# Kernel tuning notes

Measured on AMD Instinct MI355X. Metric: run time of the kernel, lower is better.

## Reference

```python
import jax, jax.numpy as jnp
import numpy as np

SOBEL = np.array([[1, 0, -1], [2, 0, -2], [1, 0, -1]], dtype=np.float32)


def _conv3(x, w):
    # 3x3 conv, stride 1, padding 1, no bias (NCHW / OIHW)
    return jax.lax.conv_general_dilated(
        x, w, window_strides=(1, 1), padding='SAME',
        dimension_numbers=('NCHW', 'OIHW', 'NCHW'))


def _sobel_conv(x, wx, wy, w1, b1):
    # |sobel_x| + |sobel_y| followed by 1x1 conv (w1: [O, C])
    e = jnp.abs(_conv3(x, wx)) + jnp.abs(_conv3(x, wy))
    return jnp.einsum('bchw,oc->bohw', e, w1) + b1[None, :, None, None]


def setup_inputs() -> dict:
    key = jax.random.key(0)
    ks = jax.random.split(key, 12)
    B, C, H, W = 2, 64, 64, 64
    dk = C // 8
    sob = jnp.asarray(SOBEL)
    inp = {
        'vi': jax.random.normal(ks[0], (B, C, H, W), jnp.float32),
        'ir': jax.random.normal(ks[1], (B, C, H, W), jnp.float32),
        # Sobel conv weights: torch copy_ broadcasts the 3x3 kernel over [C,C,3,3]
        'wsx_vi': jnp.broadcast_to(sob, (C, C, 3, 3)).copy(),
        'wsy_vi': jnp.broadcast_to(sob.T, (C, C, 3, 3)).copy(),
        'w1_vi': jax.random.normal(ks[2], (dk, C), jnp.float32) * 0.05,
        'b1_vi': jax.random.normal(ks[3], (dk,), jnp.float32) * 0.05,
        'wsx_q': jnp.broadcast_to(sob, (2 * C, 2 * C, 3, 3)).copy(),
        'wsy_q': jnp.broadcast_to(sob.T, (2 * C, 2 * C, 3, 3)).copy(),
        'w1_q': jax.random.normal(ks[4], (dk, 2 * C), jnp.float32) * 0.05,
        'b1_q': jax.random.normal(ks[5], (dk,), jnp.float32) * 0.05,
        'wsx_ir': jnp.broadcast_to(sob, (C, C, 3, 3)).copy(),
        'wsy_ir': jnp.broadcast_to(sob.T, (C, C, 3, 3)).copy(),
        'w1_ir': jax.random.normal(ks[6], (dk, C), jnp.float32) * 0.05,
        'b1_ir': jax.random.normal(ks[7], (dk,), jnp.float32) * 0.05,
        'wv_vi': jax.random.normal(ks[8], (C, C), jnp.float32) * 0.05,
        'bv_vi': jax.random.normal(ks[9], (C,), jnp.float32) * 0.05,
        'wv_ir': jax.random.normal(ks[10], (C, C), jnp.float32) * 0.05,
        'bv_ir': jax.random.normal(ks[11], (C,), jnp.float32) * 0.05,
    }
    return inp


def reference(vi, ir, wsx_vi, wsy_vi, w1_vi, b1_vi, wsx_q, wsy_q, w1_q, b1_q,
              wsx_ir, wsy_ir, w1_ir, b1_ir, wv_vi, bv_vi, wv_ir, bv_ir):
    B, C, H, W = vi.shape
    N = H * W
    # Query from concatenated modalities: [B, N, dk]
    xq = _sobel_conv(jnp.concatenate([vi, ir], axis=1), wsx_q, wsy_q, w1_q, b1_q)
    xq = xq.reshape(B, -1, N).transpose(0, 2, 1)
    # Keys: [B, dk, N]
    vi_xk = _sobel_conv(vi, wsx_vi, wsy_vi, w1_vi, b1_vi).reshape(B, -1, N)
    ir_xk = _sobel_conv(ir, wsx_ir, wsy_ir, w1_ir, b1_ir).reshape(B, -1, N)
    # Values (1x1 convs): [B, C, N]
    vi_xv = (jnp.einsum('bchw,oc->bohw', vi, wv_vi) + bv_vi[None, :, None, None]).reshape(B, C, N)
    ir_xv = (jnp.einsum('bchw,oc->bohw', ir, wv_ir) + bv_ir[None, :, None, None]).reshape(B, C, N)
    # Unscaled attention, softmax over last dim: [B, N, N]
    vi_attn = jax.nn.softmax(jnp.einsum('bnd,bdm->bnm', xq, vi_xk), axis=-1)
    ir_attn = jax.nn.softmax(jnp.einsum('bnd,bdm->bnm', xq, ir_xk), axis=-1)
    # Cross combination: vi value routed by ir attention (and vice versa)
    vi_out = jnp.einsum('bcn,bmn->bcm', vi_xv, ir_attn).reshape(B, C, H, W)
    ir_out = jnp.einsum('bcn,bmn->bcm', ir_xv, vi_attn).reshape(B, C, H, W)
    return vi_out, ir_out
```

## Files before the change

kernel.cpp:

```cpp
#include <hip/hip_runtime.h>
#include <hip/hip_bf16.h>

typedef __attribute__((ext_vector_type(8))) short bf16x8;
typedef __attribute__((ext_vector_type(4))) float f32x4;
typedef __attribute__((ext_vector_type(4))) int   i32x4;


__global__ __launch_bounds__(256) void kP_prep(
    const float* __restrict__ vi, const float* __restrict__ ir,
    const float* __restrict__ w1_vi, const float* __restrict__ w1_q,
    const float* __restrict__ b1_q,  const float* __restrict__ w1_ir,
    const float* __restrict__ wv_vi, const float* __restrict__ bv_vi,
    const float* __restrict__ wv_ir, const float* __restrict__ bv_ir,
    float* __restrict__ s, float* __restrict__ scal,
    __hip_bfloat16* __restrict__ Vc) {
    const int t = threadIdx.x;
    if (blockIdx.x < 256) {
        __shared__ __align__(16) char wlds[64 * 128];
        const int bm = blockIdx.x >> 6, nt = blockIdx.x & 63;
        const int b = bm >> 1, mod = bm & 1;
        const float* wv = mod ? wv_ir : wv_vi;
        const float* bv = mod ? bv_ir : bv_vi;
        const float* x = (mod ? ir : vi) + b * (64 * 4096);
        {
            const float* src = wv + t * 16;
            int row = t >> 2, colb = (t & 3) * 32;
            int pk[8];
            #pragma unroll
            for (int j = 0; j < 8; ++j)
                asm("v_cvt_pk_bf16_f32 %0, %1, %2" : "=v"(pk[j])
                    : "v"(src[2 * j]), "v"(src[2 * j + 1]));
            int sw = (row & 7) << 4;
            i32x4 lo = {pk[0], pk[1], pk[2], pk[3]};
            i32x4 hi = {pk[4], pk[5], pk[6], pk[7]};
            *(i32x4*)(wlds + row * 128 + (colb ^ sw)) = lo;
            *(i32x4*)(wlds + row * 128 + ((colb + 16) ^ sw)) = hi;
        }
        __syncthreads();
        const int wvid = t >> 6, lane = t & 63;
        const int col = lane & 15, g = lane >> 4;
        const int n = nt * 64 + wvid * 16 + col;
        bf16x8 afr[4][2];
        #pragma unroll
        for (int cb = 0; cb < 4; ++cb) {
            int row = cb * 16 + col;
            int sw = (row & 7) << 4;
            #pragma unroll
            for (int ks = 0; ks < 2; ++ks)
                afr[cb][ks] = *(const bf16x8*)(wlds + row * 128 + ((ks * 64 + g * 16) ^ sw));
        }
        float ssum = 0.f;
        bf16x8 bfr[2];
        #pragma unroll
        for (int ks = 0; ks < 2; ++ks) {
            const float* xr = x + (ks * 32 + g * 8) * 4096 + n;
            float v[8];
            #pragma unroll
            for (int j = 0; j < 8; ++j) { v[j] = xr[j * 4096]; ssum += v[j]; }
            int pk[4];
            #pragma unroll
            for (int j = 0; j < 4; ++j)
                asm("v_cvt_pk_bf16_f32 %0, %1, %2" : "=v"(pk[j])
                    : "v"(v[2 * j]), "v"(v[2 * j + 1]));
            i32x4 bi = {pk[0], pk[1], pk[2], pk[3]};
            bfr[ks] = __builtin_bit_cast(bf16x8, bi);
        }
        ssum += __shfl_xor(ssum, 16);
        ssum += __shfl_xor(ssum, 32);
        if (lane < 16) s[bm * 4096 + nt * 64 + wvid * 16 + lane] = ssum;

        f32x4 acc[4];
        #pragma unroll
        for (int cb = 0; cb < 4; ++cb)
            #pragma unroll
            for (int r = 0; r < 4; ++r) acc[cb][r] = bv[cb * 16 + g * 4 + r];
        #pragma unroll
        for (int ks = 0; ks < 2; ++ks)
            #pragma unroll
            for (int cb = 0; cb < 4; ++cb)
                acc[cb] = __builtin_amdgcn_mfma_f32_16x16x32_bf16(afr[cb][ks], bfr[ks], acc[cb], 0, 0, 0);
        __hip_bfloat16* outp = Vc + (size_t)(bm * 64) * 4096 + n;
        #pragma unroll
        for (int cb = 0; cb < 4; ++cb)
            #pragma unroll
            for (int r = 0; r < 4; ++r)
                outp[(cb * 16 + g * 4 + r) * 4096] = __float2bfloat16(acc[cb][r]);
    } else {
        __shared__ float Ad[8], Cv[8], Ci[8], Bq[8];
        if (t < 8) {
            float a = 0.f;
            for (int c = 0; c < 128; ++c) a += w1_q[t * 128 + c];
            float cv = 0.f, ci = 0.f;
            for (int c = 0; c < 64; ++c) { cv += w1_vi[t * 64 + c]; ci += w1_ir[t * 64 + c]; }
            Ad[t] = a; Cv[t] = cv; Ci[t] = ci; Bq[t] = b1_q[t];
        }
        __syncthreads();
        if (t == 0) {
            float av = 0, gv = 0, ai = 0, gi = 0;
            for (int d = 0; d < 8; ++d) {
                av += Ad[d] * Cv[d]; gv += Bq[d] * Cv[d];
                ai += Ad[d] * Ci[d]; gi += Bq[d] * Ci[d];
            }
            scal[0] = av; scal[1] = gv; scal[2] = ai; scal[3] = gi;
        }
    }
}

#define CH 512
#define NCH 8
__global__ __launch_bounds__(512, 2) void k4_attn(
        const float* __restrict__ s, const float* __restrict__ scal,
        const float* __restrict__ wsx_vi, const float* __restrict__ wsy_vi,
        const float* __restrict__ wsx_q,  const float* __restrict__ wsy_q,
        const float* __restrict__ wsx_ir, const float* __restrict__ wsy_ir,
        const __hip_bfloat16* __restrict__ Vc, float* __restrict__ out) {
    __shared__ __align__(16) char vbuf[2][64 * CH * 2];
    __shared__ __align__(16) float elds[4096];
    __shared__ float mm[16];
    const int mt = blockIdx.x;
    const int bw = blockIdx.y;
    const int b = bw >> 1, which = bw & 1;
    const int amod = which ? 0 : 1;
    const float* wsxa = amod ? wsx_ir : wsx_vi;
    const float* wsya = amod ? wsy_ir : wsy_vi;
    const float alpha = scal[which ? 0 : 2];
    const float gamma = scal[which ? 1 : 3];
    const short* Vg = (const short*)(Vc + (size_t)(bw * 64) * 4096);

    const int tid = threadIdx.x;
    const int wvw = tid >> 6, lane = tid & 63;
    const int h = wvw >> 2, wvt = wvw & 3;
    const int col = lane & 15, g = lane >> 4;
    const int m = mt * 64 + wvt * 16 + col;

    float* sld = (float*)vbuf[0];
    const float* sg = s + (size_t)(b * 2) * 4096;
    #pragma unroll
    for (int k = 0; k < 16; ++k) { int i = tid + k * 512; sld[i] = sg[i]; }
    __syncthreads();

    float mn = 3.0e38f, mx = 0.f;
    {
        const float* sa = sld + amod * 4096;
        #pragma unroll
        for (int k2 = 0; k2 < 8; ++k2) {
            int n = tid + k2 * 512;
            int hh = n >> 6, ww = n & 63;
            float gx = 0.f, gy = 0.f;
            #pragma unroll
            for (int di = 0; di < 3; ++di)
                #pragma unroll
                for (int dj = 0; dj < 3; ++dj) {
                    int r = hh + di - 1, c2 = ww + dj - 1;
                    bool in = (r >= 0) & (r < 64) & (c2 >= 0) & (c2 < 64);
                    float v = in ? sa[r * 64 + c2] : 0.f;
                    int kk = di * 3 + dj;
                    gx = fmaf(v, wsxa[kk], gx);
                    gy = fmaf(v, wsya[kk], gy);
                }
            float ev = fabsf(gx) + fabsf(gy);
            elds[n] = ev;
            mn = fminf(mn, ev); mx = fmaxf(mx, ev);
        }
    }
    float eq;
    {
        int ww = wvt * 16 + col;
        float gx = 0.f, gy = 0.f;
        #pragma unroll
        for (int di = 0; di < 3; ++di)
            #pragma unroll
            for (int dj = 0; dj < 3; ++dj) {
                int r = mt + di - 1, c2 = ww + dj - 1;
                bool in = (r >= 0) & (r < 64) & (c2 >= 0) & (c2 < 64);
                float v = in ? (sld[r * 64 + c2] + sld[4096 + r * 64 + c2]) : 0.f;
                int kk = di * 3 + dj;
                gx = fmaf(v, wsx_q[kk], gx);
                gy = fmaf(v, wsy_q[kk], gy);
            }
        eq = fabsf(gx) + fabsf(gy);
    }
    #pragma unroll
    for (int o = 32; o; o >>= 1) {
        mn = fminf(mn, __shfl_xor(mn, o));
        mx = fmaxf(mx, __shfl_xor(mx, o));
    }
    if (lane == 0) { mm[wvw] = mn; mm[8 + wvw] = mx; }
    __syncthreads();
    float emn = mm[0], emx = mm[8];
    #pragma unroll
    for (int w = 1; w < 8; ++w) {
        emn = fminf(emn, mm[w]); emx = fmaxf(emx, mm[8 + w]);
    }
    const float L2E = 1.4426950408889634f;
    const float t  = alpha * eq + gamma;
    const float t2 = t * L2E;
    const float nM2 = -((t > 0.f) ? t * emx : t * emn) * L2E;

    #pragma unroll
    for (int k = 0; k < 8; ++k) {
        int id = tid + k * 512;
        int c = id >> 6, ss = id & 63;
        bf16x8 v = *(const bf16x8*)(Vg + c * 4096 + ss * 8);
        *(bf16x8*)(vbuf[0] + c * 1024 + ((ss * 16) ^ ((c & 31) << 4))) = v;
    }
    __syncthreads();

    f32x4 acc[4] = {};
    f32x4 accz = {};
    bf16x8 ones;
    #pragma unroll
    for (int j = 0; j < 8; ++j) ones[j] = (short)0x3F80;

    for (int ck = 0; ck < NCH; ++ck) {
        bf16x8 stg[8];
        const bool pf = (ck + 1 < NCH);
        if (pf) {
            const short* src = Vg + (ck + 1) * CH;
            #pragma unroll
            for (int k = 0; k < 8; ++k) {
                int id = tid + k * 512;
                int c = id >> 6, ss = id & 63;
                stg[k] = *(const bf16x8*)(src + c * 4096 + ss * 8);
            }
        }
        const char* vb = vbuf[ck & 1];
        const float* el = elds + ck * CH;
        #pragma unroll
        for (int it2 = 0; it2 < 8; ++it2) {
            const int n0 = (h * 8 + it2) * 32;
            bf16x8 af[4];
            #pragma unroll
            for (int cb = 0; cb < 4; ++cb) {
                int row = cb * 16 + col;
                int byte = row * 1024 + (((n0 + g * 8) * 2) ^ ((row & 31) << 4));
                af[cb] = *(const bf16x8*)(vb + byte);
            }
            f32x4 e0 = *(const f32x4*)(el + n0 + g * 8);
            f32x4 e1 = *(const f32x4*)(el + n0 + g * 8 + 4);
            float p[8];
            #pragma unroll
            for (int j = 0; j < 4; ++j) {
                float g0 = fmaf(e0[j], t2, nM2);
                float g1 = fmaf(e1[j], t2, nM2);
                asm("v_exp_f32 %0, %1" : "=v"(p[j])     : "v"(g0));
                asm("v_exp_f32 %0, %1" : "=v"(p[j + 4]) : "v"(g1));
            }
            int pk0, pk1, pk2, pk3;
            asm("v_cvt_pk_bf16_f32 %0, %1, %2" : "=v"(pk0) : "v"(p[0]), "v"(p[1]));
            asm("v_cvt_pk_bf16_f32 %0, %1, %2" : "=v"(pk1) : "v"(p[2]), "v"(p[3]));
            asm("v_cvt_pk_bf16_f32 %0, %1, %2" : "=v"(pk2) : "v"(p[4]), "v"(p[5]));
            asm("v_cvt_pk_bf16_f32 %0, %1, %2" : "=v"(pk3) : "v"(p[6]), "v"(p[7]));
            i32x4 pki = {pk0, pk1, pk2, pk3};
            bf16x8 bfrag = __builtin_bit_cast(bf16x8, pki);
            #pragma unroll
            for (int cb = 0; cb < 4; ++cb)
                acc[cb] = __builtin_amdgcn_mfma_f32_16x16x32_bf16(af[cb], bfrag, acc[cb], 0, 0, 0);
            accz = __builtin_amdgcn_mfma_f32_16x16x32_bf16(ones, bfrag, accz, 0, 0, 0);
        }
        __syncthreads();
        if (pf) {
            char* wb = vbuf[(ck + 1) & 1];
            #pragma unroll
            for (int k = 0; k < 8; ++k) {
                int id = tid + k * 512;
                int c = id >> 6, ss = id & 63;
                *(bf16x8*)(wb + c * 1024 + ((ss * 16) ^ ((c & 31) << 4))) = stg[k];
            }
            __syncthreads();
        }
    }

    float* red = (float*)vbuf[0];
    if (h == 1) {
        int base = (wvt * 64 + lane) * 21;
        #pragma unroll
        for (int cb = 0; cb < 4; ++cb)
            *(f32x4*)(red + base + cb * 4) = acc[cb];
        red[base + 16] = accz[0];
    }
    __syncthreads();
    if (h == 0) {
        int base = (wvt * 64 + lane) * 21;
        #pragma unroll
        for (int cb = 0; cb < 4; ++cb)
            acc[cb] += *(const f32x4*)(red + base + cb * 4);
        float z = accz[0] + red[base + 16];
        float inv = 1.0f / z;
        float* ob = out + which * (2 * 64 * 4096) + b * (64 * 4096) + m;
        #pragma unroll
        for (int cb = 0; cb < 4; ++cb) {
            int c = cb * 16 + g * 4;
            #pragma unroll
            for (int r = 0; r < 4; ++r) ob[(c + r) * 4096] = acc[cb][r] * inv;
        }
    }
}

extern "C" void kernel_launch(void* const* d_in, const int* in_sizes, int n_in,
                              void* d_out, int out_size, void* d_ws, size_t ws_size,
                              hipStream_t stream) {
    const float* vi     = (const float*)d_in[0];
    const float* ir     = (const float*)d_in[1];
    const float* wsx_vi = (const float*)d_in[2];
    const float* wsy_vi = (const float*)d_in[3];
    const float* w1_vi  = (const float*)d_in[4];
    const float* wsx_q  = (const float*)d_in[6];
    const float* wsy_q  = (const float*)d_in[7];
    const float* w1_q   = (const float*)d_in[8];
    const float* b1_q   = (const float*)d_in[9];
    const float* wsx_ir = (const float*)d_in[10];
    const float* wsy_ir = (const float*)d_in[11];
    const float* w1_ir  = (const float*)d_in[12];
    const float* wv_vi  = (const float*)d_in[14];
    const float* bv_vi  = (const float*)d_in[15];
    const float* wv_ir  = (const float*)d_in[16];
    const float* bv_ir  = (const float*)d_in[17];
    (void)in_sizes; (void)n_in; (void)out_size;

    char* ws = (char*)d_ws;
    float* scal = (float*)ws;
    float* s    = (float*)(ws + 1280);
    __hip_bfloat16* Vc = (__hip_bfloat16*)(ws + 1280 + 65536);
    float* out = (float*)d_out;
    (void)ws_size;

    kP_prep<<<dim3(257), 256, 0, stream>>>(vi, ir, w1_vi, w1_q, b1_q, w1_ir,
                                           wv_vi, bv_vi, wv_ir, bv_ir, s, scal, Vc);
    k4_attn<<<dim3(64, 4), 512, 0, stream>>>(s, scal, wsx_vi, wsy_vi, wsx_q, wsy_q,
                                             wsx_ir, wsy_ir, Vc, out);
}
```

Measured before the change: 34.46 us.

## Fuse prep and attention kernels into one cooperative launch with grid sync

Merges the prep kernel (value projection, channel sums, scalar reductions) and the attention kernel into a single cooperative kernel of 256 blocks separated by a grid-wide barrier. Each block also recomputes the alpha/gamma scalars locally from w1 sums in shared memory instead of reading them from a separate workspace. The aim is to remove one kernel launch and the gap between launches. In exchange it adds grid-sync overhead, and the cooperative launch requires all 256 blocks to be resident at once.

Result: slower. 67.52 us (+96.0%).

```diff
diff --git a/kernel.cpp b/kernel.cpp
--- a/kernel.cpp
+++ b/kernel.cpp
@@ -1,30 +1,49 @@
 #include <hip/hip_runtime.h>
 #include <hip/hip_bf16.h>
+#include <hip/hip_cooperative_groups.h>
+
+namespace cg = cooperative_groups;
 
 typedef __attribute__((ext_vector_type(8))) short bf16x8;
 typedef __attribute__((ext_vector_type(4))) float f32x4;
 typedef __attribute__((ext_vector_type(4))) int   i32x4;
 
 
-__global__ __launch_bounds__(256) void kP_prep(
+#define CH 512
+#define NCH 8
+
+__global__ __launch_bounds__(512, 2) void kAll(
     const float* __restrict__ vi, const float* __restrict__ ir,
+    const float* __restrict__ wsx_vi, const float* __restrict__ wsy_vi,
+    const float* __restrict__ wsx_q,  const float* __restrict__ wsy_q,
+    const float* __restrict__ wsx_ir, const float* __restrict__ wsy_ir,
     const float* __restrict__ w1_vi, const float* __restrict__ w1_q,
     const float* __restrict__ b1_q,  const float* __restrict__ w1_ir,
     const float* __restrict__ wv_vi, const float* __restrict__ bv_vi,
     const float* __restrict__ wv_ir, const float* __restrict__ bv_ir,
-    float* __restrict__ s, float* __restrict__ scal,
-    __hip_bfloat16* __restrict__ Vc) {
-    const int t = threadIdx.x;
-    if (blockIdx.x < 256) {
-        __shared__ __align__(16) char wlds[64 * 128];
-        const int bm = blockIdx.x >> 6, nt = blockIdx.x & 63;
-        const int b = bm >> 1, mod = bm & 1;
+    float* __restrict__ s, __hip_bfloat16* __restrict__ Vc,
+    float* __restrict__ out) {
+    __shared__ __align__(16) char vbuf[2][64 * CH * 2];
+    __shared__ __align__(16) float elds[4096];
+    __shared__ float mm[16];
+    __shared__ float agA[8], agC[8], agB[8];
+
+    const int bid = blockIdx.x;
+    const int tid = threadIdx.x;
+    const int wvw = tid >> 6, lane = tid & 63;
+    const int grp = bid >> 6;
+    const int sub = bid & 63;
+    const int b = grp >> 1, which = grp & 1;
+    const int col = lane & 15, g = lane >> 4;
+
+    {
+        const int mod = which;
         const float* wv = mod ? wv_ir : wv_vi;
         const float* bv = mod ? bv_ir : bv_vi;
         const float* x = (mod ? ir : vi) + b * (64 * 4096);
-        {
-            const float* src = wv + t * 16;
-            int row = t >> 2, colb = (t & 3) * 32;
+        if (tid < 256) {
+            const float* src = wv + tid * 16;
+            int row = tid >> 2, colb = (tid & 3) * 32;
             int pk[8];
             #pragma unroll
             for (int j = 0; j < 8; ++j)
@@ -33,105 +52,96 @@
             int sw = (row & 7) << 4;
             i32x4 lo = {pk[0], pk[1], pk[2], pk[3]};
             i32x4 hi = {pk[4], pk[5], pk[6], pk[7]};
-            *(i32x4*)(wlds + row * 128 + (colb ^ sw)) = lo;
-            *(i32x4*)(wlds + row * 128 + ((colb + 16) ^ sw)) = hi;
+            *(i32x4*)(vbuf[0] + row * 128 + (colb ^ sw)) = lo;
+            *(i32x4*)(vbuf[0] + row * 128 + ((colb + 16) ^ sw)) = hi;
         }
         __syncthreads();
-        const int wvid = t >> 6, lane = t & 63;
-        const int col = lane & 15, g = lane >> 4;
-        const int n = nt * 64 + wvid * 16 + col;
-        bf16x8 afr[4][2];
-        #pragma unroll
-        for (int cb = 0; cb < 4; ++cb) {
-            int row = cb * 16 + col;
-            int sw = (row & 7) << 4;
+        if (wvw < 4) {
+            const int n = sub * 64 + wvw * 16 + col;
+            bf16x8 afr[4][2];
+            #pragma unroll
+            for (int cb = 0; cb < 4; ++cb) {
+                int row = cb * 16 + col;
+                int sw = (row & 7) << 4;
+                #pragma unroll
+                for (int ks = 0; ks < 2; ++ks)
+                    afr[cb][ks] = *(const bf16x8*)(vbuf[0] + row * 128 + ((ks * 64 + g * 16) ^ sw));
+            }
+            float ssum = 0.f;
+            bf16x8 bfr[2];
+            #pragma unroll
+            for (int ks = 0; ks < 2; ++ks) {
+                const float* xr = x + (ks * 32 + g * 8) * 4096 + n;
+                float v[8];
+                #pragma unroll
+                for (int j = 0; j < 8; ++j) { v[j] = xr[j * 4096]; ssum += v[j]; }
+                int pk[4];
+                #pragma unroll
+                for (int j = 0; j < 4; ++j)
+                    asm("v_cvt_pk_bf16_f32 %0, %1, %2" : "=v"(pk[j])
+                        : "v"(v[2 * j]), "v"(v[2 * j + 1]));
+                i32x4 bi = {pk[0], pk[1], pk[2], pk[3]};
+                bfr[ks] = __builtin_bit_cast(bf16x8, bi);
+            }
+            ssum += __shfl_xor(ssum, 16);
+            ssum += __shfl_xor(ssum, 32);
+            if (lane < 16) s[grp * 4096 + sub * 64 + wvw * 16 + lane] = ssum;
+
+            f32x4 acc[4];
+            #pragma unroll
+            for (int cb = 0; cb < 4; ++cb)
+                #pragma unroll
+                for (int r = 0; r < 4; ++r) acc[cb][r] = bv[cb * 16 + g * 4 + r];
             #pragma unroll
             for (int ks = 0; ks < 2; ++ks)
-                afr[cb][ks] = *(const bf16x8*)(wlds + row * 128 + ((ks * 64 + g * 16) ^ sw));
-        }
-        float ssum = 0.f;
-        bf16x8 bfr[2];
-        #pragma unroll
-        for (int ks = 0; ks < 2; ++ks) {
-            const float* xr = x + (ks * 32 + g * 8) * 4096 + n;
-            float v[8];
-            #pragma unroll
-            for (int j = 0; j < 8; ++j) { v[j] = xr[j * 4096]; ssum += v[j]; }
-            int pk[4];
-            #pragma unroll
-            for (int j = 0; j < 4; ++j)
-                asm("v_cvt_pk_bf16_f32 %0, %1, %2" : "=v"(pk[j])
-                    : "v"(v[2 * j]), "v"(v[2 * j + 1]));
-            i32x4 bi = {pk[0], pk[1], pk[2], pk[3]};
-            bfr[ks] = __builtin_bit_cast(bf16x8, bi);
-        }
-        ssum += __shfl_xor(ssum, 16);
-        ssum += __shfl_xor(ssum, 32);
-        if (lane < 16) s[bm * 4096 + nt * 64 + wvid * 16 + lane] = ssum;
-
-        f32x4 acc[4];
-        #pragma unroll
-        for (int cb = 0; cb < 4; ++cb)
-            #pragma unroll
-            for (int r = 0; r < 4; ++r) acc[cb][r] = bv[cb * 16 + g * 4 + r];
-        #pragma unroll
-        for (int ks = 0; ks < 2; ++ks)
+                #pragma unroll
+                for (int cb = 0; cb < 4; ++cb)
+                    acc[cb] = __builtin_amdgcn_mfma_f32_16x16x32_bf16(afr[cb][ks], bfr[ks], acc[cb], 0, 0, 0);
+            __hip_bfloat16* outp = Vc + (size_t)(grp * 64) * 4096 + n;
             #pragma unroll
             for (int cb = 0; cb < 4; ++cb)
-                acc[cb] = __builtin_amdgcn_mfma_f32_16x16x32_bf16(afr[cb][ks], bfr[ks], acc[cb], 0, 0, 0);
-        __hip_bfloat16* outp = Vc + (size_t)(bm * 64) * 4096 + n;
-        #pragma unroll
-        for (int cb = 0; cb < 4; ++cb)
-            #pragma unroll
-            for (int r = 0; r < 4; ++r)
-                outp[(cb * 16 + g * 4 + r) * 4096] = __float2bfloat16(acc[cb][r]);
-    } else {
-        __shared__ float Ad[8], Cv[8], Ci[8], Bq[8];
-        if (t < 8) {
-            float a = 0.f;
-            for (int c = 0; c < 128; ++c) a += w1_q[t * 128 + c];
-            float cv = 0.f, ci = 0.f;
-            for (int c = 0; c < 64; ++c) { cv += w1_vi[t * 64 + c]; ci += w1_ir[t * 64 + c]; }
-            Ad[t] = a; Cv[t] = cv; Ci[t] = ci; Bq[t] = b1_q[t];
+                #pragma unroll
+                for (int r = 0; r < 4; ++r)
+                    outp[(cb * 16 + g * 4 + r) * 4096] = __float2bfloat16(acc[cb][r]);
+        } else if (wvw == 4) {
+            int d = lane >> 3, i = lane & 7;
+            const float* p = w1_q + d * 128 + i * 16;
+            float v = 0.f;
+            #pragma unroll
+            for (int k = 0; k < 16; ++k) v += p[k];
+            #pragma unroll
+            for (int o = 1; o < 8; o <<= 1) v += __shfl_xor(v, o);
+            if (i == 0) agA[d] = v;
+        } else if (wvw == 5) {
+            const float* w1x = which ? w1_vi : w1_ir;
+            int d = lane >> 3, i = lane & 7;
+            const float* p = w1x + d * 64 + i * 8;
+            float v = 0.f;
+            #pragma unroll
+            for (int k = 0; k < 8; ++k) v += p[k];
+            #pragma unroll
+            for (int o = 1; o < 8; o <<= 1) v += __shfl_xor(v, o);
+            if (i == 0) agC[d] = v;
+        } else if (wvw == 6) {
+            if (lane < 8) agB[lane] = b1_q[lane];
         }
         __syncthreads();
-        if (t == 0) {
-            float av = 0, gv = 0, ai = 0, gi = 0;
-            for (int d = 0; d < 8; ++d) {
-                av += Ad[d] * Cv[d]; gv += Bq[d] * Cv[d];
-                ai += Ad[d] * Ci[d]; gi += Bq[d] * Ci[d];
-            }
-            scal[0] = av; scal[1] = gv; scal[2] = ai; scal[3] = gi;
-        }
-    }
-}
-
-#define CH 512
-#define NCH 8
-__global__ __launch_bounds__(512, 2) void k4_attn(
-        const float* __restrict__ s, const float* __restrict__ scal,
-        const float* __restrict__ wsx_vi, const float* __restrict__ wsy_vi,
-        const float* __restrict__ wsx_q,  const float* __restrict__ wsy_q,
-        const float* __restrict__ wsx_ir, const float* __restrict__ wsy_ir,
-        const __hip_bfloat16* __restrict__ Vc, float* __restrict__ out) {
-    __shared__ __align__(16) char vbuf[2][64 * CH * 2];
-    __shared__ __align__(16) float elds[4096];
-    __shared__ float mm[16];
-    const int mt = blockIdx.x;
-    const int bw = blockIdx.y;
-    const int b = bw >> 1, which = bw & 1;
+    }
+    float alpha = 0.f, gamma = 0.f;
+    #pragma unroll
+    for (int d = 0; d < 8; ++d) {
+        alpha = fmaf(agA[d], agC[d], alpha);
+        gamma = fmaf(agB[d], agC[d], gamma);
+    }
+
+    cg::this_grid().sync();
+
     const int amod = which ? 0 : 1;
     const float* wsxa = amod ? wsx_ir : wsx_vi;
     const float* wsya = amod ? wsy_ir : wsy_vi;
-    const float alpha = scal[which ? 0 : 2];
-    const float gamma = scal[which ? 1 : 3];
-    const short* Vg = (const short*)(Vc + (size_t)(bw * 64) * 4096);
-
-    const int tid = threadIdx.x;
-    const int wvw = tid >> 6, lane = tid & 63;
+    const short* Vg = (const short*)(Vc + (size_t)(grp * 64) * 4096);
     const int h = wvw >> 2, wvt = wvw & 3;
-    const int col = lane & 15, g = lane >> 4;
-    const int m = mt * 64 + wvt * 16 + col;
+    const int m = sub * 64 + wvt * 16 + col;
 
     float* sld = (float*)vbuf[0];
     const float* sg = s + (size_t)(b * 2) * 4096;
@@ -171,7 +181,7 @@
         for (int di = 0; di < 3; ++di)
             #pragma unroll
             for (int dj = 0; dj < 3; ++dj) {
-                int r = mt + di - 1, c2 = ww + dj - 1;
+                int r = sub + di - 1, c2 = ww + dj - 1;
                 bool in = (r >= 0) & (r < 64) & (c2 >= 0) & (c2 < 64);
                 float v = in ? (sld[r * 64 + c2] + sld[4096 + r * 64 + c2]) : 0.f;
                 int kk = di * 3 + dj;
@@ -319,14 +329,16 @@
     (void)in_sizes; (void)n_in; (void)out_size;
 
     char* ws = (char*)d_ws;
-    float* scal = (float*)ws;
-    float* s    = (float*)(ws + 1280);
-    __hip_bfloat16* Vc = (__hip_bfloat16*)(ws + 1280 + 65536);
+    float* s = (float*)ws;
+    __hip_bfloat16* Vc = (__hip_bfloat16*)(ws + 65536);
     float* out = (float*)d_out;
     (void)ws_size;
 
-    kP_prep<<<dim3(257), 256, 0, stream>>>(vi, ir, w1_vi, w1_q, b1_q, w1_ir,
-                                           wv_vi, bv_vi, wv_ir, bv_ir, s, scal, Vc);
-    k4_attn<<<dim3(64, 4), 512, 0, stream>>>(s, scal, wsx_vi, wsy_vi, wsx_q, wsy_q,
-                                             wsx_ir, wsy_ir, Vc, out);
+    void* args[] = { (void*)&vi, (void*)&ir,
+                     (void*)&wsx_vi, (void*)&wsy_vi, (void*)&wsx_q, (void*)&wsy_q,
+                     (void*)&wsx_ir, (void*)&wsy_ir,
+                     (void*)&w1_vi, (void*)&w1_q, (void*)&b1_q, (void*)&w1_ir,
+                     (void*)&wv_vi, (void*)&bv_vi, (void*)&wv_ir, (void*)&bv_ir,
+                     (void*)&s, (void*)&Vc, (void*)&out };
+    hipLaunchCooperativeKernel((void*)kAll, dim3(256), dim3(512), args, 0, stream);
 }
```

## Split attention n-range across all eight waves and reuse V fragments over m-groups

Applied to the files above, without the earlier changes.

In the attention kernel, the work split changes from two n-halves of four waves (each wave owning 16 query columns) to eight waves that each own a slice of n and all four 16-column m-groups. Each V fragment read from LDS now feeds four MFMA groups, cutting LDS traffic for V. The cost is more accumulator registers and a larger cross-wave reduction: eight partial sums per output, held in shared memory, instead of two. The hand-written bf16 conversion and exp asm is also replaced with compiler casts and the exp2 builtin.

New measurement: 37.66 us. 1.09x slower.

```diff
diff --git a/kernel.cpp b/kernel.cpp
--- a/kernel.cpp
+++ b/kernel.cpp
@@ -2,8 +2,15 @@
 #include <hip/hip_bf16.h>
 
 typedef __attribute__((ext_vector_type(8))) short bf16x8;
+typedef __attribute__((ext_vector_type(8))) __bf16 bf16v8;
 typedef __attribute__((ext_vector_type(4))) float f32x4;
 typedef __attribute__((ext_vector_type(4))) int   i32x4;
+
+#if __has_builtin(__builtin_amdgcn_exp2f)
+#define EXP2(x) __builtin_amdgcn_exp2f(x)
+#else
+#define EXP2(x) exp2f(x)
+#endif
 
 
 __global__ __launch_bounds__(256) void kP_prep(
@@ -25,16 +32,15 @@
         {
             const float* src = wv + t * 16;
             int row = t >> 2, colb = (t & 3) * 32;
-            int pk[8];
-            #pragma unroll
-            for (int j = 0; j < 8; ++j)
-                asm("v_cvt_pk_bf16_f32 %0, %1, %2" : "=v"(pk[j])
-                    : "v"(src[2 * j]), "v"(src[2 * j + 1]));
+            bf16v8 lo8, hi8;
+            #pragma unroll
+            for (int j = 0; j < 8; ++j) {
+                lo8[j] = (__bf16)src[j];
+                hi8[j] = (__bf16)src[8 + j];
+            }
             int sw = (row & 7) << 4;
-            i32x4 lo = {pk[0], pk[1], pk[2], pk[3]};
-            i32x4 hi = {pk[4], pk[5], pk[6], pk[7]};
-            *(i32x4*)(wlds + row * 128 + (colb ^ sw)) = lo;
-            *(i32x4*)(wlds + row * 128 + ((colb + 16) ^ sw)) = hi;
+            *(i32x4*)(wlds + row * 128 + (colb ^ sw)) = __builtin_bit_cast(i32x4, lo8);
+            *(i32x4*)(wlds + row * 128 + ((colb + 16) ^ sw)) = __builtin_bit_cast(i32x4, hi8);
         }
         __syncthreads();
         const int wvid = t >> 6, lane = t & 63;
@@ -54,16 +60,14 @@
         #pragma unroll
         for (int ks = 0; ks < 2; ++ks) {
             const float* xr = x + (ks * 32 + g * 8) * 4096 + n;
-            float v[8];
-            #pragma unroll
-            for (int j = 0; j < 8; ++j) { v[j] = xr[j * 4096]; ssum += v[j]; }
-            int pk[4];
-            #pragma unroll
-            for (int j = 0; j < 4; ++j)
-                asm("v_cvt_pk_bf16_f32 %0, %1, %2" : "=v"(pk[j])
-                    : "v"(v[2 * j]), "v"(v[2 * j + 1]));
-            i32x4 bi = {pk[0], pk[1], pk[2], pk[3]};
-            bfr[ks] = __builtin_bit_cast(bf16x8, bi);
+            bf16v8 pb;
+            #pragma unroll
+            for (int j = 0; j < 8; ++j) {
+                float v = xr[j * 4096];
+                ssum += v;
+                pb[j] = (__bf16)v;
+            }
+            bfr[ks] = __builtin_bit_cast(bf16x8, pb);
         }
         ssum += __shfl_xor(ssum, 16);
         ssum += __shfl_xor(ssum, 32);
@@ -114,9 +118,11 @@
         const float* __restrict__ wsx_q,  const float* __restrict__ wsy_q,
         const float* __restrict__ wsx_ir, const float* __restrict__ wsy_ir,
         const __hip_bfloat16* __restrict__ Vc, float* __restrict__ out) {
-    __shared__ __align__(16) char vbuf[2][64 * CH * 2];
-    __shared__ __align__(16) float elds[4096];
+    __shared__ __align__(16) char smem[147456];
     __shared__ float mm[16];
+    char* vbuf0 = smem;
+    char* vbuf1 = smem + 65536;
+    float* elds = (float*)(smem + 131072);
     const int mt = blockIdx.x;
     const int bw = blockIdx.y;
     const int b = bw >> 1, which = bw & 1;
@@ -129,11 +135,9 @@
 
     const int tid = threadIdx.x;
     const int wvw = tid >> 6, lane = tid & 63;
-    const int h = wvw >> 2, wvt = wvw & 3;
     const int col = lane & 15, g = lane >> 4;
-    const int m = mt * 64 + wvt * 16 + col;
-
-    float* sld = (float*)vbuf[0];
+
+    float* sld = (float*)vbuf0;
     const float* sg = s + (size_t)(b * 2) * 4096;
     #pragma unroll
     for (int k = 0; k < 16; ++k) { int i = tid + k * 512; sld[i] = sg[i]; }
@@ -163,9 +167,10 @@
             mn = fminf(mn, ev); mx = fmaxf(mx, ev);
         }
     }
-    float eq;
-    {
-        int ww = wvt * 16 + col;
+    float eq[4];
+    #pragma unroll
+    for (int mg = 0; mg < 4; ++mg) {
+        int ww = mg * 16 + col;
         float gx = 0.f, gy = 0.f;
         #pragma unroll
         for (int di = 0; di < 3; ++di)
@@ -178,7 +183,7 @@
                 gx = fmaf(v, wsx_q[kk], gx);
                 gy = fmaf(v, wsy_q[kk], gy);
             }
-        eq = fabsf(gx) + fabsf(gy);
+        eq[mg] = fabsf(gx) + fabsf(gy);
     }
     #pragma unroll
     for (int o = 32; o; o >>= 1) {
@@ -193,21 +198,25 @@
         emn = fminf(emn, mm[w]); emx = fmaxf(emx, mm[8 + w]);
     }
     const float L2E = 1.4426950408889634f;
-    const float t  = alpha * eq + gamma;
-    const float t2 = t * L2E;
-    const float nM2 = -((t > 0.f) ? t * emx : t * emn) * L2E;
+    float t2[4], nM2[4];
+    #pragma unroll
+    for (int mg = 0; mg < 4; ++mg) {
+        float t = alpha * eq[mg] + gamma;
+        t2[mg]  = t * L2E;
+        nM2[mg] = -((t > 0.f) ? t * emx : t * emn) * L2E;
+    }
 
     #pragma unroll
     for (int k = 0; k < 8; ++k) {
         int id = tid + k * 512;
         int c = id >> 6, ss = id & 63;
         bf16x8 v = *(const bf16x8*)(Vg + c * 4096 + ss * 8);
-        *(bf16x8*)(vbuf[0] + c * 1024 + ((ss * 16) ^ ((c & 31) << 4))) = v;
+        *(bf16x8*)(vbuf0 + c * 1024 + ((ss * 16) ^ ((c & 31) << 4))) = v;
     }
     __syncthreads();
 
-    f32x4 acc[4] = {};
-    f32x4 accz = {};
+    f32x4 acc[4][4] = {};
+    f32x4 accz[4] = {};
     bf16x8 ones;
     #pragma unroll
     for (int j = 0; j < 8; ++j) ones[j] = (short)0x3F80;
@@ -224,11 +233,11 @@
                 stg[k] = *(const bf16x8*)(src + c * 4096 + ss * 8);
             }
         }
-        const char* vb = vbuf[ck & 1];
+        const char* vb = (ck & 1) ? vbuf1 : vbuf0;
         const float* el = elds + ck * CH;
         #pragma unroll
-        for (int it2 = 0; it2 < 8; ++it2) {
-            const int n0 = (h * 8 + it2) * 32;
+        for (int j = 0; j < 2; ++j) {
+            const int n0 = (wvw * 2 + j) * 32;
             bf16x8 af[4];
             #pragma unroll
             for (int cb = 0; cb < 4; ++cb) {
@@ -238,29 +247,26 @@
             }
             f32x4 e0 = *(const f32x4*)(el + n0 + g * 8);
             f32x4 e1 = *(const f32x4*)(el + n0 + g * 8 + 4);
-            float p[8];
-            #pragma unroll
-            for (int j = 0; j < 4; ++j) {
-                float g0 = fmaf(e0[j], t2, nM2);
-                float g1 = fmaf(e1[j], t2, nM2);
-                asm("v_exp_f32 %0, %1" : "=v"(p[j])     : "v"(g0));
-                asm("v_exp_f32 %0, %1" : "=v"(p[j + 4]) : "v"(g1));
-            }
-            int pk0, pk1, pk2, pk3;
-            asm("v_cvt_pk_bf16_f32 %0, %1, %2" : "=v"(pk0) : "v"(p[0]), "v"(p[1]));
-            asm("v_cvt_pk_bf16_f32 %0, %1, %2" : "=v"(pk1) : "v"(p[2]), "v"(p[3]));
-            asm("v_cvt_pk_bf16_f32 %0, %1, %2" : "=v"(pk2) : "v"(p[4]), "v"(p[5]));
-            asm("v_cvt_pk_bf16_f32 %0, %1, %2" : "=v"(pk3) : "v"(p[6]), "v"(p[7]));
-            i32x4 pki = {pk0, pk1, pk2, pk3};
-            bf16x8 bfrag = __builtin_bit_cast(bf16x8, pki);
-            #pragma unroll
-            for (int cb = 0; cb < 4; ++cb)
-                acc[cb] = __builtin_amdgcn_mfma_f32_16x16x32_bf16(af[cb], bfrag, acc[cb], 0, 0, 0);
-            accz = __builtin_amdgcn_mfma_f32_16x16x32_bf16(ones, bfrag, accz, 0, 0, 0);
+            #pragma unroll
+            for (int mg = 0; mg < 4; ++mg) {
+                bf16v8 pb;
+                #pragma unroll
+                for (int q = 0; q < 4; ++q) {
+                    float g0 = fmaf(e0[q], t2[mg], nM2[mg]);
+                    float g1 = fmaf(e1[q], t2[mg], nM2[mg]);
+                    pb[q]     = (__bf16)EXP2(g0);
+                    pb[q + 4] = (__bf16)EXP2(g1);
+                }
+                bf16x8 bfrag = __builtin_bit_cast(bf16x8, pb);
+                #pragma unroll
+                for (int cb = 0; cb < 4; ++cb)
+                    acc[mg][cb] = __builtin_amdgcn_mfma_f32_16x16x32_bf16(af[cb], bfrag, acc[mg][cb], 0, 0, 0);
+                accz[mg] = __builtin_amdgcn_mfma_f32_16x16x32_bf16(ones, bfrag, accz[mg], 0, 0, 0);
+            }
         }
         __syncthreads();
         if (pf) {
-            char* wb = vbuf[(ck + 1) & 1];
+            char* wb = (ck & 1) ? vbuf0 : vbuf1;
             #pragma unroll
             for (int k = 0; k < 8; ++k) {
                 int id = tid + k * 512;
@@ -271,29 +277,36 @@
         }
     }
 
-    float* red = (float*)vbuf[0];
-    if (h == 1) {
-        int base = (wvt * 64 + lane) * 21;
+    float* rbuf = (float*)smem;
+    #pragma unroll
+    for (int mg = 0; mg < 4; ++mg) {
+        int base = ((wvw * 4 + mg) * 64 + lane) * 17;
         #pragma unroll
         for (int cb = 0; cb < 4; ++cb)
-            *(f32x4*)(red + base + cb * 4) = acc[cb];
-        red[base + 16] = accz[0];
+            *(f32x4*)(rbuf + base + cb * 4) = acc[mg][cb];
+        rbuf[base + 16] = accz[mg][0];
     }
     __syncthreads();
-    if (h == 0) {
-        int base = (wvt * 64 + lane) * 21;
-        #pragma unroll
-        for (int cb = 0; cb < 4; ++cb)
-            acc[cb] += *(const f32x4*)(red + base + cb * 4);
-        float z = accz[0] + red[base + 16];
+    {
+        const int mg = wvw & 3, hh = wvw >> 2;
+        f32x4 sum0 = {}, sum1 = {};
+        float z = 0.f;
+        #pragma unroll
+        for (int src = 0; src < 8; ++src) {
+            int sb = ((src * 4 + mg) * 64 + lane) * 17;
+            sum0 += *(const f32x4*)(rbuf + sb + (hh * 2 + 0) * 4);
+            sum1 += *(const f32x4*)(rbuf + sb + (hh * 2 + 1) * 4);
+            z += rbuf[sb + 16];
+        }
         float inv = 1.0f / z;
+        int m = mt * 64 + mg * 16 + col;
         float* ob = out + which * (2 * 64 * 4096) + b * (64 * 4096) + m;
-        #pragma unroll
-        for (int cb = 0; cb < 4; ++cb) {
-            int c = cb * 16 + g * 4;
-            #pragma unroll
-            for (int r = 0; r < 4; ++r) ob[(c + r) * 4096] = acc[cb][r] * inv;
-        }
+        int c0 = (hh * 2) * 16 + g * 4;
+        int c1 = (hh * 2 + 1) * 16 + g * 4;
+        #pragma unroll
+        for (int r = 0; r < 4; ++r) ob[(c0 + r) * 4096] = sum0[r] * inv;
+        #pragma unroll
+        for (int r = 0; r < 4; ++r) ob[(c1 + r) * 4096] = sum1[r] * inv;
     }
 }
 
```
